# Optimization experiments

Measured on AMD Instinct MI355X. Metric: run time of the kernel, lower is better.

## Reference

```python
import jax, jax.numpy as jnp
import numpy as np

B, C, T, E = 8, 64, 128, 256
TYPE_NUM, NF = 40, 128
KS = (5, 4, 3)
NEG = -1e10


def setup_inputs() -> dict:
    key = jax.random.key(0)
    ks = jax.random.split(key, 10)
    s = 0.02
    return {
        "query": jax.random.normal(ks[0], (C, E), jnp.float32),
        "context": jax.random.normal(ks[1], (B, T, E), jnp.float32),
        "mask": jax.random.randint(ks[2], (B, T), 0, 2, jnp.int32),
        "W_hidden": jax.random.normal(ks[3], (4 * E, 4 * E), jnp.float32) * s,
        "b_hidden": jnp.zeros((4 * E,), jnp.float32),
        "W_v": jax.random.normal(ks[4], (1, 4 * E), jnp.float32) * s,
        "b_v": jnp.zeros((1,), jnp.float32),
        "W_lin": jax.random.normal(ks[5], (E, 4 * E), jnp.float32) * s,
        "b_lin": jnp.zeros((E,), jnp.float32),
        "conv_w0": jax.random.normal(ks[6], (NF, E, KS[0]), jnp.float32) * s,
        "conv_b0": jnp.zeros((NF,), jnp.float32),
        "conv_w1": jax.random.normal(ks[7], (NF, E, KS[1]), jnp.float32) * s,
        "conv_b1": jnp.zeros((NF,), jnp.float32),
        "conv_w2": jax.random.normal(ks[8], (NF, E, KS[2]), jnp.float32) * s,
        "conv_b2": jnp.zeros((NF,), jnp.float32),
        "W_cnn": jax.random.normal(ks[9], (TYPE_NUM, NF * 3), jnp.float32) * s,
        "b_cnn": jnp.zeros((TYPE_NUM,), jnp.float32),
    }


def _pair_feat(a, b):
    # [.., e] x2 -> [.., 4e]: [a, b, |a-b|, a*b]
    return jnp.concatenate([a, b, jnp.abs(a - b), a * b], axis=-1)


def _conv1d(x, w, b):
    # x: [b, e, c], w: [f, e, k] (torch Conv1d layout) -> [b, f, c-k+1]
    y = jax.lax.conv_general_dilated(
        x, w, window_strides=(1,), padding="VALID",
        dimension_numbers=("NCH", "OIH", "NCH"))
    return y + b[None, :, None]


def reference(query, context, mask, W_hidden, b_hidden, W_v, b_v,
              W_lin, b_lin, conv_w0, conv_b0, conv_w1, conv_b1,
              conv_w2, conv_b2, W_cnn, b_cnn):
    b, t, e = context.shape
    c = query.shape[0]
    q_ = jnp.broadcast_to(query[None, :, None, :], (b, c, t, e))
    ctx_ = jnp.broadcast_to(context[:, None, :, :], (b, c, t, e))
    feat = _pair_feat(q_, ctx_)                                 # [b,c,t,4e]
    h = jnp.tanh(feat @ W_hidden.T + b_hidden)                  # [b,c,t,4e]
    scores = (h @ W_v.T + b_v)[..., 0]                          # [b,c,t]
    scores = jnp.where((mask < 1)[:, None, :], NEG, scores)
    attn = jax.nn.softmax(scores, axis=-1)                      # [b,c,t]
    g = jnp.einsum("bct,bte->bce", attn, context)               # [b,c,e]
    q2 = jnp.broadcast_to(query[None], (b, c, e))
    h2 = jnp.tanh(_pair_feat(q2, g) @ W_hidden.T + b_hidden)    # [b,c,4e]
    x = h2 @ W_lin.T + b_lin                                    # [b,c,e]
    xT = jnp.transpose(x, (0, 2, 1))                            # [b,e,c]
    pooled = []
    for w, bb in ((conv_w0, conv_b0), (conv_w1, conv_b1), (conv_w2, conv_b2)):
        y = jax.nn.relu(_conv1d(xT, w, bb))                     # [b,f,c-k+1]
        pooled.append(jnp.max(y, axis=2))                       # [b,f]
    cnn = jnp.concatenate(pooled, axis=1)                       # [b,3f]
    return cnn @ W_cnn.T + b_cnn                                # [b,type_num]
```

## Files before the change

kernel.cpp:

```cpp
#include <hip/hip_runtime.h>
#include <math.h>


typedef __bf16 bf16x8 __attribute__((ext_vector_type(8)));
typedef float  f32x4  __attribute__((ext_vector_type(4)));

__device__ __forceinline__ float ftanh(float v) {
    float t = __expf(2.f * v);
    return 1.f - 2.f * __builtin_amdgcn_rcpf(t + 1.f);
}

__device__ __forceinline__ void gld_lds16(const __bf16* g, __bf16* l) {
    __builtin_amdgcn_global_load_lds(
        (const __attribute__((address_space(1))) void*)g,
        (__attribute__((address_space(3))) void*)l, 16, 0, 0);
}

__global__ __launch_bounds__(256) void cvt_kernel(
    const float* __restrict__ Wh, const float* __restrict__ Wl,
    const float* __restrict__ ctx,
    const float* __restrict__ cw0, const float* __restrict__ cw1,
    const float* __restrict__ cw2,
    const float* __restrict__ q, const float* __restrict__ bh,
    float* __restrict__ Apre, float* __restrict__ x,
    __bf16* __restrict__ Whbf, __bf16* __restrict__ Whbf_t,
    __bf16* __restrict__ Wlbf, __bf16* __restrict__ ctxbf,
    float* __restrict__ wt0, float* __restrict__ wt1,
    float* __restrict__ wt2, float* __restrict__ gsc,
    float* __restrict__ cnn)
{
    if (blockIdx.x < 16) {
        __shared__ float As[16][68];
        __shared__ float Bs[16][68];
        const int tid = threadIdx.x;
        const int n0 = blockIdx.x * 64;
        const int tm = tid >> 4, tn = tid & 15;
        const int lr = tid >> 2;
        const int lc = (tid & 3) * 4;

        float acc[4][4];
#pragma unroll
        for (int i = 0; i < 4; ++i)
#pragma unroll
            for (int j = 0; j < 4; ++j) acc[i][j] = 0.f;

        for (int k0 = 0; k0 < 256; k0 += 16) {
            float4 av = *reinterpret_cast<const float4*>(q + (size_t)lr * 256 + k0 + lc);
            float4 bv = *reinterpret_cast<const float4*>(Wh + (size_t)(n0 + lr) * 1024 + k0 + lc);
            As[lc + 0][lr] = av.x; As[lc + 1][lr] = av.y; As[lc + 2][lr] = av.z; As[lc + 3][lr] = av.w;
            Bs[lc + 0][lr] = bv.x; Bs[lc + 1][lr] = bv.y; Bs[lc + 2][lr] = bv.z; Bs[lc + 3][lr] = bv.w;
            __syncthreads();
#pragma unroll
            for (int kk = 0; kk < 16; ++kk) {
                float4 a = *reinterpret_cast<const float4*>(&As[kk][tm * 4]);
                float4 b = *reinterpret_cast<const float4*>(&Bs[kk][tn * 4]);
                float ar[4] = {a.x, a.y, a.z, a.w};
                float br[4] = {b.x, b.y, b.z, b.w};
#pragma unroll
                for (int i = 0; i < 4; ++i)
#pragma unroll
                    for (int j = 0; j < 4; ++j) acc[i][j] += ar[i] * br[j];
            }
            __syncthreads();
        }

#pragma unroll
        for (int i = 0; i < 4; ++i) {
            int m = tm * 4 + i;
            float vals[4];
#pragma unroll
            for (int j = 0; j < 4; ++j) vals[j] = acc[i][j] + bh[n0 + tn * 4 + j];
            float4 o; o.x = vals[0]; o.y = vals[1]; o.z = vals[2]; o.w = vals[3];
            *reinterpret_cast<float4*>(Apre + (size_t)m * 1024 + n0 + tn * 4) = o;
        }
        return;
    }

    int idx = (blockIdx.x - 16) * 256 + threadIdx.x;
    if (idx < 131072) {
        const float* s = Wh + (size_t)idx * 8;
        float4 f0 = *reinterpret_cast<const float4*>(s);
        float4 f1 = *reinterpret_cast<const float4*>(s + 4);
        bf16x8 u;
        u[0] = (__bf16)f0.x; u[1] = (__bf16)f0.y; u[2] = (__bf16)f0.z; u[3] = (__bf16)f0.w;
        u[4] = (__bf16)f1.x; u[5] = (__bf16)f1.y; u[6] = (__bf16)f1.z; u[7] = (__bf16)f1.w;
        *reinterpret_cast<bf16x8*>(Whbf + (size_t)idx * 8) = u;
        return;
    }
    if (idx < 196608) {
        int di = idx - 131072;
        int ng = di >> 13, kc = (di >> 10) & 7;
        int row = (di >> 3) & 127, kgp = di & 7;
        int kg = kgp ^ (row & 7);
        const float* s = Wh + (size_t)(ng * 128 + row) * 1024 + 512 + kc * 64 + kg * 8;
        float4 f0 = *reinterpret_cast<const float4*>(s);
        float4 f1 = *reinterpret_cast<const float4*>(s + 4);
        bf16x8 u;
        u[0] = (__bf16)f0.x; u[1] = (__bf16)f0.y; u[2] = (__bf16)f0.z; u[3] = (__bf16)f0.w;
        u[4] = (__bf16)f1.x; u[5] = (__bf16)f1.y; u[6] = (__bf16)f1.z; u[7] = (__bf16)f1.w;
        *reinterpret_cast<bf16x8*>(Whbf_t + (size_t)di * 8) = u;
        return;
    }
    if (idx < 229376) {
        int di = idx - 196608;
        const float* s = Wl + (size_t)di * 8;
        float4 f0 = *reinterpret_cast<const float4*>(s);
        float4 f1 = *reinterpret_cast<const float4*>(s + 4);
        bf16x8 u;
        u[0] = (__bf16)f0.x; u[1] = (__bf16)f0.y; u[2] = (__bf16)f0.z; u[3] = (__bf16)f0.w;
        u[4] = (__bf16)f1.x; u[5] = (__bf16)f1.y; u[6] = (__bf16)f1.z; u[7] = (__bf16)f1.w;
        *reinterpret_cast<bf16x8*>(Wlbf + (size_t)di * 8) = u;
        return;
    }
    if (idx < 262144) {
        int di = idx - 229376;
        const float* s = ctx + (size_t)di * 8;
        float4 f0 = *reinterpret_cast<const float4*>(s);
        float4 f1 = *reinterpret_cast<const float4*>(s + 4);
        bf16x8 u;
        u[0] = (__bf16)f0.x; u[1] = (__bf16)f0.y; u[2] = (__bf16)f0.z; u[3] = (__bf16)f0.w;
        u[4] = (__bf16)f1.x; u[5] = (__bf16)f1.y; u[6] = (__bf16)f1.z; u[7] = (__bf16)f1.w;
        *reinterpret_cast<bf16x8*>(ctxbf + (size_t)di * 8) = u;
        return;
    }
    if (idx < 425984) {
        int j = idx - 262144; int f = j & 127, rest = j >> 7;
        int i = rest % 5, e = rest / 5;
        wt0[j] = cw0[(size_t)(f * 256 + e) * 5 + i]; return;
    }
    if (idx < 557056) {
        int j = idx - 425984; int f = j & 127, rest = j >> 7;
        int i = rest & 3, e = rest >> 2;
        wt1[j] = cw1[(size_t)(f * 256 + e) * 4 + i]; return;
    }
    if (idx < 655360) {
        int j = idx - 557056; int f = j & 127, rest = j >> 7;
        int i = rest % 3, e = rest / 3;
        wt2[j] = cw2[(size_t)(f * 256 + e) * 3 + i]; return;
    }
    if (idx < 671744) {
        int di = idx - 655360;
        reinterpret_cast<float4*>(gsc)[di] = (float4){0.f, 0.f, 0.f, 0.f};
        return;
    }
    if (idx < 674816) { cnn[idx - 671744] = 0.f; return; }
    if (idx < 707584) {
        int di = idx - 674816;
        reinterpret_cast<float4*>(x)[di] = (float4){0.f, 0.f, 0.f, 0.f};
    }
}

__global__ __launch_bounds__(512, 4) void attn_mfma_kernel(
    const float* __restrict__ q,
    const float* __restrict__ ctx,
    const __bf16* __restrict__ Whbf_t,
    const float* __restrict__ Wv,
    const float* __restrict__ Apre,
    const float* __restrict__ Bpre,
    float* __restrict__ gsc)
{
    __shared__ __bf16 Us[256 * 64];
    __shared__ __bf16 Ws[128 * 64];
    __shared__ float qc[512];
    __shared__ float sc[256];

    const int tid = threadIdx.x;
    const int cpair = blockIdx.x >> 3, ng = blockIdx.x & 7;
    const int b = cpair >> 5, c0 = (cpair & 31) * 2;
    const int wave = tid >> 6, lane = tid & 63;
    const int w1 = wave & 1, w0 = wave >> 1;
    const int m0 = w0 * 64;
    const int l15 = lane & 15, quad = lane >> 4;
    const int swz = l15 & 7;
    const int kg = tid & 7;

    qc[tid] = q[(size_t)(c0 + (tid >> 8)) * 256 + (tid & 255)];
    if (tid < 256) sc[tid] = 0.f;
    __syncthreads();

    f32x4 acc[4][4];
#pragma unroll
    for (int mi = 0; mi < 4; ++mi)
#pragma unroll
        for (int ni = 0; ni < 4; ++ni) acc[mi][ni] = (f32x4){0.f, 0.f, 0.f, 0.f};

    for (int kc = 0; kc < 8; ++kc) {
        const bool isabs = (kc < 4);
        const int e0 = (kc & 3) * 64;
        const int eb = e0 + kg * 8;
        float qA[8], qB[8];
#pragma unroll
        for (int i = 0; i < 8; ++i) { qA[i] = qc[eb + i]; qB[i] = qc[256 + eb + i]; }
        bf16x8 u0[2], u1[2];
#pragma unroll
        for (int it = 0; it < 2; ++it) {
            const int trow = it * 64 + (tid >> 3);
            const float* cp = ctx + (size_t)(b * 128 + trow) * 256 + eb;
            float4 cl0 = *reinterpret_cast<const float4*>(cp);
            float4 cl1 = *reinterpret_cast<const float4*>(cp + 4);
            float cv[8] = {cl0.x, cl0.y, cl0.z, cl0.w, cl1.x, cl1.y, cl1.z, cl1.w};
#pragma unroll
            for (int i = 0; i < 8; ++i) {
                u0[it][i] = (__bf16)(isabs ? fabsf(qA[i] - cv[i]) : qA[i] * cv[i]);
                u1[it][i] = (__bf16)(isabs ? fabsf(qB[i] - cv[i]) : qB[i] * cv[i]);
            }
        }
        __syncthreads();
        const __bf16* wtile = Whbf_t + (size_t)(ng * 8 + kc) * 8192;
#pragma unroll
        for (int it = 0; it < 2; ++it) {
            int gidx = wave * 128 + it * 64;
            gld_lds16(wtile + (size_t)(gidx + lane) * 8, &Ws[gidx * 8]);
        }
#pragma unroll
        for (int it = 0; it < 2; ++it) {
            const int trow = it * 64 + (tid >> 3);
            const int off = (kg ^ (trow & 7)) * 8;
            *reinterpret_cast<bf16x8*>(&Us[trow * 64 + off]) = u0[it];
            *reinterpret_cast<bf16x8*>(&Us[(trow + 128) * 64 + off]) = u1[it];
        }
        __syncthreads();
#pragma unroll
        for (int ks = 0; ks < 2; ++ks) {
            const int c8 = (((ks * 4 + quad) ^ swz)) * 8;
            bf16x8 a[4], bfr[4];
#pragma unroll
            for (int mi = 0; mi < 4; ++mi)
                a[mi] = *reinterpret_cast<const bf16x8*>(
                    &Us[(m0 + mi * 16 + l15) * 64 + c8]);
#pragma unroll
            for (int ni = 0; ni < 4; ++ni)
                bfr[ni] = *reinterpret_cast<const bf16x8*>(
                    &Ws[(w1 * 64 + ni * 16 + l15) * 64 + c8]);
#pragma unroll
            for (int mi = 0; mi < 4; ++mi)
#pragma unroll
                for (int ni = 0; ni < 4; ++ni)
                    acc[mi][ni] = __builtin_amdgcn_mfma_f32_16x16x32_bf16(
                        a[mi], bfr[ni], acc[mi][ni], 0, 0, 0);
        }
    }

    const int jcol = ng * 128 + w1 * 64 + l15;
    const int c = c0 + (w0 >> 1);
    float av[4], wv[4];
#pragma unroll
    for (int ni = 0; ni < 4; ++ni) {
        av[ni] = Apre[(size_t)c * 1024 + jcol + ni * 16];
        wv[ni] = Wv[jcol + ni * 16];
    }
#pragma unroll
    for (int mi = 0; mi < 4; ++mi) {
        const int tb = (w0 & 1) * 64 + mi * 16 + quad * 4;
        float p[4];
#pragma unroll
        for (int r = 0; r < 4; ++r) {
            const float* bp = Bpre + (size_t)(b * 128 + tb + r) * 1024 + jcol;
            float s = 0.f;
#pragma unroll
            for (int ni = 0; ni < 4; ++ni)
                s += ftanh(acc[mi][ni][r] + av[ni] + bp[ni * 16]) * wv[ni];
            p[r] = s;
        }
#pragma unroll
        for (int off = 1; off < 16; off <<= 1)
#pragma unroll
            for (int r = 0; r < 4; ++r) p[r] += __shfl_xor(p[r], off, 16);
        if (l15 == 0) {
#pragma unroll
            for (int r = 0; r < 4; ++r)
                atomicAdd(&sc[(w0 >> 1) * 128 + tb + r], p[r]);
        }
    }
    __syncthreads();

    if (tid < 256) atomicAdd(&gsc[(size_t)(b * 64 + c0) * 128 + tid], sc[tid]);
}

__global__ __launch_bounds__(256) void attn_tail_kernel(
    const float* __restrict__ ctx, const int* __restrict__ mask,
    const float* __restrict__ bv, const float* __restrict__ gsc,
    const float* __restrict__ q, __bf16* __restrict__ feat2)
{
    __shared__ float sc[128];
    __shared__ float red;
    const int tid = threadIdx.x;
    const int bc = blockIdx.x, b = bc >> 6, c = bc & 63;

    if (tid < 128) {
        float s = gsc[(size_t)bc * 128 + tid] + bv[0];
        if (mask[b * 128 + tid] < 1) s = -1e10f;
        sc[tid] = s;
    }
    __syncthreads();
    if (tid < 64) {
        float m = fmaxf(sc[tid], sc[tid + 64]);
        for (int off = 32; off; off >>= 1) m = fmaxf(m, __shfl_xor(m, off, 64));
        if (tid == 0) red = m;
    }
    __syncthreads();
    const float mx = red;
    if (tid < 128) sc[tid] = __expf(sc[tid] - mx);
    __syncthreads();
    if (tid < 64) {
        float s = sc[tid] + sc[tid + 64];
        for (int off = 32; off; off >>= 1) s += __shfl_xor(s, off, 64);
        if (tid == 0) red = s;
    }
    __syncthreads();
    const float inv = 1.f / red;

    float gv = 0.f;
    for (int t = 0; t < 128; ++t) gv += sc[t] * ctx[(size_t)(b * 128 + t) * 256 + tid];
    gv *= inv;
    const float qv = q[(size_t)c * 256 + tid];
    __bf16* o = feat2 + (size_t)bc * 768 + tid;
    o[0]   = (__bf16)gv;
    o[256] = (__bf16)fabsf(qv - gv);
    o[512] = (__bf16)(qv * gv);
}

template <int ACT, int OUTBF, int BMODE, int ATOMIC>
__global__ __launch_bounds__(256) void mfma_gemm_kernel(
    const __bf16* __restrict__ A, int lda,
    const __bf16* __restrict__ B, int ldb,
    const float* __restrict__ bias, void* __restrict__ Cout,
    int K, int ldc)
{
    __shared__ __bf16 As[64 * 72];
    __shared__ __bf16 Bs[64 * 72];
    const int tid = threadIdx.x;
    const int wave = tid >> 6, lane = tid & 63;
    const int w0 = wave >> 1, w1 = wave & 1;
    const int l15 = lane & 15, quad = lane >> 4;
    const int m0 = blockIdx.y * 64, n0 = blockIdx.x * 64;

    int kbeg = 0, kend = K;
    if (ATOMIC) {
        int kchunk = K / gridDim.z;
        kbeg = blockIdx.z * kchunk;
        kend = kbeg + kchunk;
    }

    f32x4 acc[2][2];
#pragma unroll
    for (int mi = 0; mi < 2; ++mi)
#pragma unroll
        for (int ni = 0; ni < 2; ++ni) acc[mi][ni] = (f32x4){0.f, 0.f, 0.f, 0.f};

    for (int k0 = kbeg; k0 < kend; k0 += 64) {
        __syncthreads();
#pragma unroll
        for (int it = 0; it < 2; ++it) {
            int idx = tid + it * 256;
            int row = idx >> 3, kgi = idx & 7;
            int4 va = *reinterpret_cast<const int4*>(A + (size_t)(m0 + row) * lda + k0 + kgi * 8);
            *reinterpret_cast<int4*>(&As[row * 72 + kgi * 8]) = va;
            int4 vb = *reinterpret_cast<const int4*>(B + (size_t)(n0 + row) * ldb + k0 + kgi * 8);
            *reinterpret_cast<int4*>(&Bs[row * 72 + kgi * 8]) = vb;
        }
        __syncthreads();
#pragma unroll
        for (int ks = 0; ks < 2; ++ks) {
            bf16x8 a[2], bb[2];
#pragma unroll
            for (int mi = 0; mi < 2; ++mi)
                a[mi] = *reinterpret_cast<const bf16x8*>(
                    &As[(w0 * 32 + mi * 16 + l15) * 72 + ks * 32 + quad * 8]);
#pragma unroll
            for (int ni = 0; ni < 2; ++ni)
                bb[ni] = *reinterpret_cast<const bf16x8*>(
                    &Bs[(w1 * 32 + ni * 16 + l15) * 72 + ks * 32 + quad * 8]);
#pragma unroll
            for (int mi = 0; mi < 2; ++mi)
#pragma unroll
                for (int ni = 0; ni < 2; ++ni)
                    acc[mi][ni] = __builtin_amdgcn_mfma_f32_16x16x32_bf16(
                        a[mi], bb[ni], acc[mi][ni], 0, 0, 0);
        }
    }

#pragma unroll
    for (int mi = 0; mi < 2; ++mi)
#pragma unroll
        for (int ni = 0; ni < 2; ++ni) {
            int col = n0 + w1 * 32 + ni * 16 + l15;
#pragma unroll
            for (int r = 0; r < 4; ++r) {
                int row = m0 + w0 * 32 + mi * 16 + quad * 4 + r;
                float bsv = (BMODE == 0) ? bias[col]
                          : (BMODE == 1) ? bias[(row & 63) * 1024 + col] : 0.f;
                if (ATOMIC) {
                    float v = acc[mi][ni][r] + (blockIdx.z == 0 ? bsv : 0.f);
                    atomicAdd((float*)Cout + (size_t)row * ldc + col, v);
                } else {
                    float v = acc[mi][ni][r] + bsv;
                    if (ACT) v = ftanh(v);
                    if (OUTBF) ((__bf16*)Cout)[(size_t)row * ldc + col] = (__bf16)v;
                    else       ((float*)Cout)[(size_t)row * ldc + col] = v;
                }
            }
        }
}

template <int KW>
__device__ __forceinline__ void conv_body(
    const float* __restrict__ x, const float* __restrict__ wt,
    float* __restrict__ part, int b, int chunk, int bi_part, int pbase, float* xs)
{
    const int tid = threadIdx.x;
    const int f = tid & 127, esub = tid >> 7;
    const int e0 = chunk * 64;

#pragma unroll
    for (int it = 0; it < 16; ++it) {
        int idx = tid + it * 256;
        int e = idx & 63, p = idx >> 6;
        xs[e * 72 + p] = x[(size_t)(b * 64 + p) * 256 + e0 + e];
    }
    __syncthreads();

    float acc[32];
#pragma unroll
    for (int p = 0; p < 32; ++p) acc[p] = 0.f;

    for (int ei = 0; ei < 32; ++ei) {
        const int eL = esub * 32 + ei;
        float wreg[KW];
#pragma unroll
        for (int i = 0; i < KW; ++i)
            wreg[i] = wt[(size_t)((e0 + eL) * KW + i) * 128 + f];
        float xv[36];
#pragma unroll
        for (int k4 = 0; k4 < 9; ++k4) {
            float4 v = *reinterpret_cast<const float4*>(&xs[eL * 72 + pbase + k4 * 4]);
            xv[k4 * 4 + 0] = v.x; xv[k4 * 4 + 1] = v.y;
            xv[k4 * 4 + 2] = v.z; xv[k4 * 4 + 3] = v.w;
        }
#pragma unroll
        for (int i = 0; i < KW; ++i)
#pragma unroll
            for (int p = 0; p < 32; ++p)
                acc[p] = fmaf(wreg[i], xv[p + i], acc[p]);
    }

    float* op = part + ((size_t)(bi_part * 2 + esub)) * 8192 + f;
#pragma unroll
    for (int p = 0; p < 32; ++p) op[(pbase + p) * 128] = acc[p];
}

__global__ __launch_bounds__(256) void conv_partial_kernel(
    const float* __restrict__ x,
    const float* __restrict__ wt0, const float* __restrict__ wt1,
    const float* __restrict__ wt2, float* __restrict__ part)
{
    __shared__ float xs[64 * 72];
    const int bi = blockIdx.x;
    const int kw = bi >> 6, b = (bi >> 3) & 7, chunk = (bi >> 1) & 3;
    const int pbase = (bi & 1) * 32;
    const int bi_part = kw * 32 + b * 4 + chunk;
    if (kw == 0)      conv_body<5>(x, wt0, part, b, chunk, bi_part, pbase, xs);
    else if (kw == 1) conv_body<4>(x, wt1, part, b, chunk, bi_part, pbase, xs);
    else              conv_body<3>(x, wt2, part, b, chunk, bi_part, pbase, xs);
}

__global__ __launch_bounds__(128) void reduce_pool_kernel(
    const float* __restrict__ part,
    const float* __restrict__ b0, const float* __restrict__ b1,
    const float* __restrict__ b2, float* __restrict__ cnn)
{
    const int bi = blockIdx.x;
    const int kw = bi >> 6, b = (bi >> 3) & 7, pc = bi & 7;
    const int f = threadIdx.x;
    const int KW = 5 - kw, P = 64 - KW + 1;
    const float bias = (kw == 0 ? b0 : kw == 1 ? b1 : b2)[f];
    float mx = 0.f;
#pragma unroll
    for (int pl = 0; pl < 8; ++pl) {
        int p = pc * 8 + pl;
        if (p < P) {
            float s = 0.f;
#pragma unroll
            for (int c4 = 0; c4 < 4; ++c4)
#pragma unroll
                for (int es = 0; es < 2; ++es)
                    s += part[((size_t)((kw * 32 + b * 4 + c4) * 2 + es)) * 8192 + p * 128 + f];
            s += bias;
            mx = fmaxf(mx, s);
        }
    }
    if (mx > 0.f)
        atomicMax((int*)(cnn + b * 384 + kw * 128 + f), __float_as_int(mx));
}

__global__ void final_kernel(const float* __restrict__ cnn, const float* __restrict__ Wc,
                             const float* __restrict__ bc, float* __restrict__ out)
{
    int o = threadIdx.x;
    if (o >= 320) return;
    int b = o / 40, t = o - b * 40;
    float s = bc[t];
    for (int i = 0; i < 384; ++i) s += cnn[b * 384 + i] * Wc[t * 384 + i];
    out[o] = s;
}

extern "C" void kernel_launch(void* const* d_in, const int* in_sizes, int n_in,
                              void* d_out, int out_size, void* d_ws, size_t ws_size,
                              hipStream_t stream)
{
    (void)in_sizes; (void)n_in; (void)out_size; (void)ws_size;
    const float* q    = (const float*)d_in[0];
    const float* ctx  = (const float*)d_in[1];
    const int*   mask = (const int*)d_in[2];
    const float* Wh   = (const float*)d_in[3];
    const float* bh   = (const float*)d_in[4];
    const float* Wv   = (const float*)d_in[5];
    const float* bv   = (const float*)d_in[6];
    const float* Wl   = (const float*)d_in[7];
    const float* bl   = (const float*)d_in[8];
    const float* cw0  = (const float*)d_in[9];
    const float* cb0  = (const float*)d_in[10];
    const float* cw1  = (const float*)d_in[11];
    const float* cb1  = (const float*)d_in[12];
    const float* cw2  = (const float*)d_in[13];
    const float* cb2  = (const float*)d_in[14];
    const float* Wc   = (const float*)d_in[15];
    const float* bc   = (const float*)d_in[16];

    float* ws   = (float*)d_ws;
    float* Apre = ws;
    float* g    = Apre + 65536;
    float* x    = g + 131072;
    float* cnn  = x + 131072;
    float* part = cnn + 3072;
    float* wt0  = part + 1572864;
    float* wt1  = wt0 + 163840;
    float* wt2  = wt1 + 131072;
    __bf16* bfb    = (__bf16*)(wt2 + 98304);
    __bf16* Whbf   = bfb;
    __bf16* Wlbf   = bfb + 1048576;
    __bf16* feat2b = bfb + 1310720;
    __bf16* h2b    = bfb + 1703936;
    float*  gsc    = (float*)(bfb + 2228224);
    __bf16* Whbf_t = (__bf16*)part;
    __bf16* ctxbf  = Whbf_t + 524288;
    float*  Bpre   = (float*)(ctxbf + 262144);

    dim3 blk(256);
    cvt_kernel<<<2780, blk, 0, stream>>>(Wh, Wl, ctx, cw0, cw1, cw2, q, bh, Apre, x,
                                         Whbf, Whbf_t, Wlbf, ctxbf, wt0, wt1, wt2,
                                         gsc, cnn);
    mfma_gemm_kernel<0, 0, 2, 0><<<dim3(16, 16), blk, 0, stream>>>(
        ctxbf, 256, Whbf + 256, 1024, nullptr, Bpre, 256, 1024);
    attn_mfma_kernel<<<2048, dim3(512), 0, stream>>>(q, ctx, Whbf_t, Wv, Apre, Bpre, gsc);
    attn_tail_kernel<<<512, blk, 0, stream>>>(ctx, mask, bv, gsc, q, feat2b);
    mfma_gemm_kernel<1, 1, 1, 0><<<dim3(16, 8), blk, 0, stream>>>(
        feat2b, 768, Whbf + 256, 1024, Apre, h2b, 768, 1024);
    mfma_gemm_kernel<0, 0, 0, 1><<<dim3(4, 8, 4), blk, 0, stream>>>(
        h2b, 1024, Wlbf, 1024, bl, x, 1024, 256);
    conv_partial_kernel<<<192, blk, 0, stream>>>(x, wt0, wt1, wt2, part);
    reduce_pool_kernel<<<192, dim3(128), 0, stream>>>(part, cb0, cb1, cb2, cnn);
    final_kernel<<<1, 320, 0, stream>>>(cnn, Wc, bc, (float*)d_out);
}
```

Baseline: 279.2 us.

## Fuse Bpre GEMM into cvt kernel and split-K the h2 GEMM with deferred tanh

The context-by-W_hidden projection (Bpre) now runs inside the conversion kernel, which converts fp32 to bf16 on the fly, so the separate ctxbf conversion and one GEMM launch are gone. The h2 GEMM becomes a split-K atomic GEMM writing fp32 pre-activations into a buffer that attn_tail zeroes. The W_lin GEMM then applies tanh and the bf16 cast while loading its A tile. This trades two launches and an intermediate bf16 buffer for atomic traffic and redundant tanh work across N tiles.

```diff
diff --git a/kernel.cpp b/kernel.cpp
--- a/kernel.cpp
+++ b/kernel.cpp
@@ -14,6 +14,13 @@
     __builtin_amdgcn_global_load_lds(
         (const __attribute__((address_space(1))) void*)g,
         (__attribute__((address_space(3))) void*)l, 16, 0, 0);
+}
+
+__device__ __forceinline__ bf16x8 cvt8(float4 f0, float4 f1) {
+    bf16x8 u;
+    u[0] = (__bf16)f0.x; u[1] = (__bf16)f0.y; u[2] = (__bf16)f0.z; u[3] = (__bf16)f0.w;
+    u[4] = (__bf16)f1.x; u[5] = (__bf16)f1.y; u[6] = (__bf16)f1.z; u[7] = (__bf16)f1.w;
+    return u;
 }
 
 __global__ __launch_bounds__(256) void cvt_kernel(
@@ -22,18 +29,21 @@
     const float* __restrict__ cw0, const float* __restrict__ cw1,
     const float* __restrict__ cw2,
     const float* __restrict__ q, const float* __restrict__ bh,
-    float* __restrict__ Apre, float* __restrict__ x,
+    float* __restrict__ Apre, float* __restrict__ x, float* __restrict__ Bpre,
     __bf16* __restrict__ Whbf, __bf16* __restrict__ Whbf_t,
-    __bf16* __restrict__ Wlbf, __bf16* __restrict__ ctxbf,
+    __bf16* __restrict__ Wlbf,
     float* __restrict__ wt0, float* __restrict__ wt1,
     float* __restrict__ wt2, float* __restrict__ gsc,
     float* __restrict__ cnn)
 {
-    if (blockIdx.x < 16) {
-        __shared__ float As[16][68];
-        __shared__ float Bs[16][68];
-        const int tid = threadIdx.x;
-        const int n0 = blockIdx.x * 64;
+    __shared__ __align__(16) char smem[18432];
+    const int bx = blockIdx.x;
+    const int tid = threadIdx.x;
+
+    if (bx < 16) {
+        float (*As)[68] = reinterpret_cast<float(*)[68]>(smem);
+        float (*Bs)[68] = reinterpret_cast<float(*)[68]>(smem + 4352);
+        const int n0 = bx * 64;
         const int tm = tid >> 4, tn = tid & 15;
         const int lr = tid >> 2;
         const int lc = (tid & 3) * 4;
@@ -76,15 +86,77 @@
         return;
     }
 
-    int idx = (blockIdx.x - 16) * 256 + threadIdx.x;
+    if (bx < 272) {
+        __bf16* As = reinterpret_cast<__bf16*>(smem);
+        __bf16* Bs = As + 64 * 72;
+        const int bid = bx - 16;
+        const int m0 = (bid >> 4) * 64, n0 = (bid & 15) * 64;
+        const int wave = tid >> 6, lane = tid & 63;
+        const int w0 = wave >> 1, w1 = wave & 1;
+        const int l15 = lane & 15, quad = lane >> 4;
+
+        f32x4 acc[2][2];
+#pragma unroll
+        for (int mi = 0; mi < 2; ++mi)
+#pragma unroll
+            for (int ni = 0; ni < 2; ++ni) acc[mi][ni] = (f32x4){0.f, 0.f, 0.f, 0.f};
+
+        for (int k0 = 0; k0 < 256; k0 += 64) {
+            __syncthreads();
+#pragma unroll
+            for (int it = 0; it < 2; ++it) {
+                int idx = tid + it * 256;
+                int row = idx >> 3, kgi = idx & 7;
+                const float* sa = ctx + (size_t)(m0 + row) * 256 + k0 + kgi * 8;
+                float4 a0 = *reinterpret_cast<const float4*>(sa);
+                float4 a1 = *reinterpret_cast<const float4*>(sa + 4);
+                *reinterpret_cast<bf16x8*>(&As[row * 72 + kgi * 8]) = cvt8(a0, a1);
+                const float* sb = Wh + (size_t)(n0 + row) * 1024 + 256 + k0 + kgi * 8;
+                float4 b0 = *reinterpret_cast<const float4*>(sb);
+                float4 b1 = *reinterpret_cast<const float4*>(sb + 4);
+                *reinterpret_cast<bf16x8*>(&Bs[row * 72 + kgi * 8]) = cvt8(b0, b1);
+            }
+            __syncthreads();
+#pragma unroll
+            for (int ks = 0; ks < 2; ++ks) {
+                bf16x8 a[2], bb[2];
+#pragma unroll
+                for (int mi = 0; mi < 2; ++mi)
+                    a[mi] = *reinterpret_cast<const bf16x8*>(
+                        &As[(w0 * 32 + mi * 16 + l15) * 72 + ks * 32 + quad * 8]);
+#pragma unroll
+                for (int ni = 0; ni < 2; ++ni)
+                    bb[ni] = *reinterpret_cast<const bf16x8*>(
+                        &Bs[(w1 * 32 + ni * 16 + l15) * 72 + ks * 32 + quad * 8]);
+#pragma unroll
+                for (int mi = 0; mi < 2; ++mi)
+#pragma unroll
+                    for (int ni = 0; ni < 2; ++ni)
+                        acc[mi][ni] = __builtin_amdgcn_mfma_f32_16x16x32_bf16(
+                            a[mi], bb[ni], acc[mi][ni], 0, 0, 0);
+            }
+        }
+
+#pragma unroll
+        for (int mi = 0; mi < 2; ++mi)
+#pragma unroll
+            for (int ni = 0; ni < 2; ++ni) {
+                int col = n0 + w1 * 32 + ni * 16 + l15;
+#pragma unroll
+                for (int r = 0; r < 4; ++r) {
+                    int row = m0 + w0 * 32 + mi * 16 + quad * 4 + r;
+                    Bpre[(size_t)row * 1024 + col] = acc[mi][ni][r];
+                }
+            }
+        return;
+    }
+
+    int idx = (bx - 272) * 256 + tid;
     if (idx < 131072) {
         const float* s = Wh + (size_t)idx * 8;
         float4 f0 = *reinterpret_cast<const float4*>(s);
         float4 f1 = *reinterpret_cast<const float4*>(s + 4);
-        bf16x8 u;
-        u[0] = (__bf16)f0.x; u[1] = (__bf16)f0.y; u[2] = (__bf16)f0.z; u[3] = (__bf16)f0.w;
-        u[4] = (__bf16)f1.x; u[5] = (__bf16)f1.y; u[6] = (__bf16)f1.z; u[7] = (__bf16)f1.w;
-        *reinterpret_cast<bf16x8*>(Whbf + (size_t)idx * 8) = u;
+        *reinterpret_cast<bf16x8*>(Whbf + (size_t)idx * 8) = cvt8(f0, f1);
         return;
     }
     if (idx < 196608) {
@@ -95,10 +167,7 @@
         const float* s = Wh + (size_t)(ng * 128 + row) * 1024 + 512 + kc * 64 + kg * 8;
         float4 f0 = *reinterpret_cast<const float4*>(s);
         float4 f1 = *reinterpret_cast<const float4*>(s + 4);
-        bf16x8 u;
-        u[0] = (__bf16)f0.x; u[1] = (__bf16)f0.y; u[2] = (__bf16)f0.z; u[3] = (__bf16)f0.w;
-        u[4] = (__bf16)f1.x; u[5] = (__bf16)f1.y; u[6] = (__bf16)f1.z; u[7] = (__bf16)f1.w;
-        *reinterpret_cast<bf16x8*>(Whbf_t + (size_t)di * 8) = u;
+        *reinterpret_cast<bf16x8*>(Whbf_t + (size_t)di * 8) = cvt8(f0, f1);
         return;
     }
     if (idx < 229376) {
@@ -106,46 +175,32 @@
         const float* s = Wl + (size_t)di * 8;
         float4 f0 = *reinterpret_cast<const float4*>(s);
         float4 f1 = *reinterpret_cast<const float4*>(s + 4);
-        bf16x8 u;
-        u[0] = (__bf16)f0.x; u[1] = (__bf16)f0.y; u[2] = (__bf16)f0.z; u[3] = (__bf16)f0.w;
-        u[4] = (__bf16)f1.x; u[5] = (__bf16)f1.y; u[6] = (__bf16)f1.z; u[7] = (__bf16)f1.w;
-        *reinterpret_cast<bf16x8*>(Wlbf + (size_t)di * 8) = u;
+        *reinterpret_cast<bf16x8*>(Wlbf + (size_t)di * 8) = cvt8(f0, f1);
         return;
     }
-    if (idx < 262144) {
-        int di = idx - 229376;
-        const float* s = ctx + (size_t)di * 8;
-        float4 f0 = *reinterpret_cast<const float4*>(s);
-        float4 f1 = *reinterpret_cast<const float4*>(s + 4);
-        bf16x8 u;
-        u[0] = (__bf16)f0.x; u[1] = (__bf16)f0.y; u[2] = (__bf16)f0.z; u[3] = (__bf16)f0.w;
-        u[4] = (__bf16)f1.x; u[5] = (__bf16)f1.y; u[6] = (__bf16)f1.z; u[7] = (__bf16)f1.w;
-        *reinterpret_cast<bf16x8*>(ctxbf + (size_t)di * 8) = u;
-        return;
-    }
-    if (idx < 425984) {
-        int j = idx - 262144; int f = j & 127, rest = j >> 7;
+    if (idx < 393216) {
+        int j = idx - 229376; int f = j & 127, rest = j >> 7;
         int i = rest % 5, e = rest / 5;
         wt0[j] = cw0[(size_t)(f * 256 + e) * 5 + i]; return;
     }
-    if (idx < 557056) {
-        int j = idx - 425984; int f = j & 127, rest = j >> 7;
+    if (idx < 524288) {
+        int j = idx - 393216; int f = j & 127, rest = j >> 7;
         int i = rest & 3, e = rest >> 2;
         wt1[j] = cw1[(size_t)(f * 256 + e) * 4 + i]; return;
     }
-    if (idx < 655360) {
-        int j = idx - 557056; int f = j & 127, rest = j >> 7;
+    if (idx < 622592) {
+        int j = idx - 524288; int f = j & 127, rest = j >> 7;
         int i = rest % 3, e = rest / 3;
         wt2[j] = cw2[(size_t)(f * 256 + e) * 3 + i]; return;
     }
-    if (idx < 671744) {
-        int di = idx - 655360;
+    if (idx < 638976) {
+        int di = idx - 622592;
         reinterpret_cast<float4*>(gsc)[di] = (float4){0.f, 0.f, 0.f, 0.f};
         return;
     }
-    if (idx < 674816) { cnn[idx - 671744] = 0.f; return; }
-    if (idx < 707584) {
-        int di = idx - 674816;
+    if (idx < 642048) { cnn[idx - 638976] = 0.f; return; }
+    if (idx < 674816) {
+        int di = idx - 642048;
         reinterpret_cast<float4*>(x)[di] = (float4){0.f, 0.f, 0.f, 0.f};
     }
 }
@@ -280,12 +335,16 @@
 __global__ __launch_bounds__(256) void attn_tail_kernel(
     const float* __restrict__ ctx, const int* __restrict__ mask,
     const float* __restrict__ bv, const float* __restrict__ gsc,
-    const float* __restrict__ q, __bf16* __restrict__ feat2)
+    const float* __restrict__ q, __bf16* __restrict__ feat2,
+    float* __restrict__ h2pre)
 {
     __shared__ float sc[128];
     __shared__ float red;
     const int tid = threadIdx.x;
     const int bc = blockIdx.x, b = bc >> 6, c = bc & 63;
+
+    reinterpret_cast<float4*>(h2pre)[(size_t)bc * 256 + tid] =
+        (float4){0.f, 0.f, 0.f, 0.f};
 
     if (tid < 128) {
         float s = gsc[(size_t)bc * 128 + tid] + bv[0];
@@ -311,6 +370,7 @@
     const float inv = 1.f / red;
 
     float gv = 0.f;
+#pragma unroll 16
     for (int t = 0; t < 128; ++t) gv += sc[t] * ctx[(size_t)(b * 128 + t) * 256 + tid];
     gv *= inv;
     const float qv = q[(size_t)c * 256 + tid];
@@ -320,9 +380,9 @@
     o[512] = (__bf16)(qv * gv);
 }
 
-template <int ACT, int OUTBF, int BMODE, int ATOMIC>
+template <int ACT, int OUTBF, int BMODE, int ATOMIC, int ATANH>
 __global__ __launch_bounds__(256) void mfma_gemm_kernel(
-    const __bf16* __restrict__ A, int lda,
+    const void* __restrict__ A, int lda,
     const __bf16* __restrict__ B, int ldb,
     const float* __restrict__ bias, void* __restrict__ Cout,
     int K, int ldc)
@@ -354,8 +414,21 @@
         for (int it = 0; it < 2; ++it) {
             int idx = tid + it * 256;
             int row = idx >> 3, kgi = idx & 7;
-            int4 va = *reinterpret_cast<const int4*>(A + (size_t)(m0 + row) * lda + k0 + kgi * 8);
-            *reinterpret_cast<int4*>(&As[row * 72 + kgi * 8]) = va;
+            if (ATANH) {
+                const float* sa = (const float*)A + (size_t)(m0 + row) * lda + k0 + kgi * 8;
+                float4 a0 = *reinterpret_cast<const float4*>(sa);
+                float4 a1 = *reinterpret_cast<const float4*>(sa + 4);
+                bf16x8 u;
+                u[0] = (__bf16)ftanh(a0.x); u[1] = (__bf16)ftanh(a0.y);
+                u[2] = (__bf16)ftanh(a0.z); u[3] = (__bf16)ftanh(a0.w);
+                u[4] = (__bf16)ftanh(a1.x); u[5] = (__bf16)ftanh(a1.y);
+                u[6] = (__bf16)ftanh(a1.z); u[7] = (__bf16)ftanh(a1.w);
+                *reinterpret_cast<bf16x8*>(&As[row * 72 + kgi * 8]) = u;
+            } else {
+                int4 va = *reinterpret_cast<const int4*>(
+                    (const __bf16*)A + (size_t)(m0 + row) * lda + k0 + kgi * 8);
+                *reinterpret_cast<int4*>(&As[row * 72 + kgi * 8]) = va;
+            }
             int4 vb = *reinterpret_cast<const int4*>(B + (size_t)(n0 + row) * ldb + k0 + kgi * 8);
             *reinterpret_cast<int4*>(&Bs[row * 72 + kgi * 8]) = vb;
         }
@@ -540,24 +613,22 @@
     __bf16* Whbf   = bfb;
     __bf16* Wlbf   = bfb + 1048576;
     __bf16* feat2b = bfb + 1310720;
-    __bf16* h2b    = bfb + 1703936;
     float*  gsc    = (float*)(bfb + 2228224);
     __bf16* Whbf_t = (__bf16*)part;
-    __bf16* ctxbf  = Whbf_t + 524288;
-    float*  Bpre   = (float*)(ctxbf + 262144);
+    float*  Bpre   = (float*)(Whbf_t + 524288);
+    float*  h2pre  = Bpre;
 
     dim3 blk(256);
-    cvt_kernel<<<2780, blk, 0, stream>>>(Wh, Wl, ctx, cw0, cw1, cw2, q, bh, Apre, x,
-                                         Whbf, Whbf_t, Wlbf, ctxbf, wt0, wt1, wt2,
+    cvt_kernel<<<2908, blk, 0, stream>>>(Wh, Wl, ctx, cw0, cw1, cw2, q, bh,
+                                         Apre, x, Bpre,
+                                         Whbf, Whbf_t, Wlbf, wt0, wt1, wt2,
                                          gsc, cnn);
-    mfma_gemm_kernel<0, 0, 2, 0><<<dim3(16, 16), blk, 0, stream>>>(
-        ctxbf, 256, Whbf + 256, 1024, nullptr, Bpre, 256, 1024);
     attn_mfma_kernel<<<2048, dim3(512), 0, stream>>>(q, ctx, Whbf_t, Wv, Apre, Bpre, gsc);
-    attn_tail_kernel<<<512, blk, 0, stream>>>(ctx, mask, bv, gsc, q, feat2b);
-    mfma_gemm_kernel<1, 1, 1, 0><<<dim3(16, 8), blk, 0, stream>>>(
-        feat2b, 768, Whbf + 256, 1024, Apre, h2b, 768, 1024);
-    mfma_gemm_kernel<0, 0, 0, 1><<<dim3(4, 8, 4), blk, 0, stream>>>(
-        h2b, 1024, Wlbf, 1024, bl, x, 1024, 256);
+    attn_tail_kernel<<<512, blk, 0, stream>>>(ctx, mask, bv, gsc, q, feat2b, h2pre);
+    mfma_gemm_kernel<0, 0, 1, 1, 0><<<dim3(16, 8, 2), blk, 0, stream>>>(
+        feat2b, 768, Whbf + 256, 1024, Apre, h2pre, 768, 1024);
+    mfma_gemm_kernel<0, 0, 0, 1, 1><<<dim3(4, 8, 4), blk, 0, stream>>>(
+        h2pre, 1024, Wlbf, 1024, bl, x, 1024, 256);
     conv_partial_kernel<<<192, blk, 0, stream>>>(x, wt0, wt1, wt2, part);
     reduce_pool_kernel<<<192, dim3(128), 0, stream>>>(part, cb0, cb1, cb2, cnn);
     final_kernel<<<1, 320, 0, stream>>>(cnn, Wc, bc, (float*)d_out);
```

Result: faster. 273.1 us (median of 2 runs) (-2.2%).
